# Optimization experiments

Measured on AMD Instinct MI355X. Metric: run time of the kernel, lower is better.

The kernel has to match this reference:

```python
import jax, jax.numpy as jnp
import numpy as np

N_NODES = 100000
N_EDGES = 600000
N_GRAPHS = 5000
IN_DIM = 11
HID = 128
EDGE_DIM = 3
N_REST = 4  # layers 1..4
BN_EPS = 1e-5


def setup_inputs() -> dict:
    key = jax.random.key(0)
    ks = iter(jax.random.split(key, 40))
    s = 0.05
    inp = {}
    inp['x'] = jax.random.normal(next(ks), (N_NODES, IN_DIM), dtype=jnp.float32)
    inp['edge_attr'] = jax.random.normal(next(ks), (N_EDGES, EDGE_DIM), dtype=jnp.float32)
    # layer 0 (input_dim -> hidden)
    inp['e_w0'] = jax.random.normal(next(ks), (EDGE_DIM, IN_DIM), dtype=jnp.float32) * s
    inp['e_b0'] = jnp.zeros((IN_DIM,), jnp.float32)
    inp['w1_0'] = jax.random.normal(next(ks), (IN_DIM, HID), dtype=jnp.float32) * s
    inp['b1_0'] = jnp.zeros((HID,), jnp.float32)
    inp['w2_0'] = jax.random.normal(next(ks), (HID, HID), dtype=jnp.float32) * s
    inp['b2_0'] = jnp.zeros((HID,), jnp.float32)
    inp['gamma0'] = jnp.ones((HID,), jnp.float32)
    inp['beta0'] = jnp.zeros((HID,), jnp.float32)
    inp['eps0'] = jnp.zeros((), jnp.float32)
    # layers 1..4 stacked
    inp['e_w'] = jax.random.normal(next(ks), (N_REST, EDGE_DIM, HID), dtype=jnp.float32) * s
    inp['e_b'] = jnp.zeros((N_REST, HID), jnp.float32)
    inp['w1'] = jax.random.normal(next(ks), (N_REST, HID, HID), dtype=jnp.float32) * s
    inp['b1'] = jnp.zeros((N_REST, HID), jnp.float32)
    inp['w2'] = jax.random.normal(next(ks), (N_REST, HID, HID), dtype=jnp.float32) * s
    inp['b2'] = jnp.zeros((N_REST, HID), jnp.float32)
    inp['gamma'] = jnp.ones((N_REST, HID), jnp.float32)
    inp['beta'] = jnp.zeros((N_REST, HID), jnp.float32)
    inp['eps_r'] = jnp.zeros((N_REST,), jnp.float32)
    # head MLP
    inp['hw1'] = jax.random.normal(next(ks), (HID, HID), dtype=jnp.float32) * s
    inp['hb1'] = jnp.zeros((HID,), jnp.float32)
    inp['hw2'] = jax.random.normal(next(ks), (HID, HID), dtype=jnp.float32) * s
    inp['hb2'] = jnp.zeros((HID,), jnp.float32)
    inp['hw3'] = jax.random.normal(next(ks), (HID, 1), dtype=jnp.float32) * s
    inp['hb3'] = jnp.zeros((1,), jnp.float32)
    # graph structure (int constants)
    inp['edge_index'] = jax.random.randint(next(ks), (2, N_EDGES), 0, N_NODES, dtype=jnp.int32)
    inp['batch'] = jnp.sort(jax.random.randint(next(ks), (N_NODES,), 0, N_GRAPHS, dtype=jnp.int32))
    return inp


def _gine_layer(x, src, dst, edge_attr, e_w, e_b, eps, w1, b1, w2, b2, gamma, beta):
    # message = relu(x_j + Linear(edge_attr)); aggregate = scatter-add on dst
    msg = jax.nn.relu(x[src] + edge_attr @ e_w + e_b)            # [E, d]
    aggr = jax.ops.segment_sum(msg, dst, num_segments=N_NODES)  # [N, d]
    h = (1.0 + eps) * x + aggr
    h = jax.nn.relu(h @ w1 + b1) @ w2 + b2                       # GIN MLP
    mu = h.mean(axis=0)
    var = h.var(axis=0)  # biased, as torch BN training-mode normalization
    h = (h - mu) * jax.lax.rsqrt(var + BN_EPS) * gamma + beta
    return jax.nn.relu(h)


def reference(x, edge_attr, e_w0, e_b0, w1_0, b1_0, w2_0, b2_0, gamma0, beta0, eps0,
              e_w, e_b, w1, b1, w2, b2, gamma, beta, eps_r,
              hw1, hb1, hw2, hb2, hw3, hb3, edge_index, batch):
    src, dst = edge_index[0], edge_index[1]
    # layer 0: input_dim -> hidden, no residual (dims differ)
    h = _gine_layer(x, src, dst, edge_attr, e_w0, e_b0, eps0,
                    w1_0, b1_0, w2_0, b2_0, gamma0, beta0)
    # layers 1..4: hidden -> hidden, with residual
    for i in range(N_REST):
        h_res = h
        h = _gine_layer(h, src, dst, edge_attr, e_w[i], e_b[i], eps_r[i],
                        w1[i], b1[i], w2[i], b2[i], gamma[i], beta[i])
        h = h + h_res
    # global mean pool per graph
    sums = jax.ops.segment_sum(h, batch, num_segments=N_GRAPHS)
    cnts = jax.ops.segment_sum(jnp.ones((h.shape[0],), h.dtype), batch, num_segments=N_GRAPHS)
    pooled = sums / jnp.maximum(cnts, 1.0)[:, None]
    # head MLP (dropout = eval no-op)
    z = jax.nn.relu(pooled @ hw1 + hb1)
    z = jax.nn.relu(z @ hw2 + hb2)
    return z @ hw3 + hb3
```

## Files before the change

### kernel.cpp

```cpp
#include <hip/hip_runtime.h>
#include <hip/hip_fp16.h>

#define N_NODES 100000
#define N_EDGES 600000
#define N_GRAPHS 5000
#define IN_DIM 11
#define HID 128
#define NREST 4
#define BN_EPS 1e-5f
#define SCAN_BS 256
#define NBLK ((N_NODES + SCAN_BS - 1) / SCAN_BS)
#define WSLOT 16384

typedef __bf16 bf16x8 __attribute__((ext_vector_type(8)));
typedef float f32x4 __attribute__((ext_vector_type(4)));

__device__ inline bf16x8 as_bf16x8(uint4 u) { return __builtin_bit_cast(bf16x8, u); }

__device__ inline void split_bf16(float x, unsigned short& hi, unsigned short& lo) {
    unsigned int b = __float_as_uint(x);
    hi = (unsigned short)(b >> 16);
    float rem = x - __uint_as_float(b & 0xFFFF0000u);
    lo = (unsigned short)(__float_as_uint(rem) >> 16);
}

__device__ inline uint4 pack8(const unsigned short* h) {
    uint4 u;
    u.x = (unsigned)h[0] | ((unsigned)h[1] << 16);
    u.y = (unsigned)h[2] | ((unsigned)h[3] << 16);
    u.z = (unsigned)h[4] | ((unsigned)h[5] << 16);
    u.w = (unsigned)h[6] | ((unsigned)h[7] << 16);
    return u;
}

__global__ void k_zero(int* deg, int* gstart, int* gend, float* stats) {
    int i = blockIdx.x * 256 + threadIdx.x;
    if (i < N_NODES) deg[i] = 0;
    if (i < N_GRAPHS) { gstart[i] = 0; gend[i] = 0; }
    if (i < 5 * 2 * HID) stats[i] = 0.f;
}

__global__ void k_deg(const int* __restrict__ ei, int* __restrict__ deg) {
    int e = blockIdx.x * 256 + threadIdx.x;
    if (e < N_EDGES) atomicAdd(&deg[ei[N_EDGES + e]], 1);
}

__global__ void k_scan_a(const int* __restrict__ deg, int* __restrict__ rowstart,
                         int* __restrict__ bsum) {
    __shared__ int sh[SCAN_BS];
    int t = threadIdx.x, i = blockIdx.x * SCAN_BS + t;
    int v = (i < N_NODES) ? deg[i] : 0;
    sh[t] = v;
    __syncthreads();
    for (int off = 1; off < SCAN_BS; off <<= 1) {
        int add = (t >= off) ? sh[t - off] : 0;
        __syncthreads();
        sh[t] += add;
        __syncthreads();
    }
    if (i < N_NODES) rowstart[i] = sh[t] - v;
    if (t == SCAN_BS - 1) bsum[blockIdx.x] = sh[t];
}

__global__ void k_scan_b(const int* __restrict__ bsum, int* __restrict__ boff) {
    __shared__ int sh[512];
    int t = threadIdx.x;
    int v = (t < NBLK) ? bsum[t] : 0;
    sh[t] = v;
    __syncthreads();
    for (int off = 1; off < 512; off <<= 1) {
        int add = (t >= off) ? sh[t - off] : 0;
        __syncthreads();
        sh[t] += add;
        __syncthreads();
    }
    if (t < NBLK) boff[t] = sh[t] - v;
}

__global__ void k_scan_c(int* __restrict__ rowstart, const int* __restrict__ boff,
                         int* __restrict__ cur) {
    int i = blockIdx.x * 256 + threadIdx.x;
    if (i < N_NODES) {
        int v = rowstart[i] + boff[i / SCAN_BS];
        rowstart[i] = v;
        cur[i] = v;
    }
    if (i == 0) rowstart[N_NODES] = N_EDGES;
}

__global__ void k_fill(const int* __restrict__ ei, const float* __restrict__ ea,
                       int* __restrict__ cur, int* __restrict__ csr_src,
                       float* __restrict__ csr_ea) {
    int e = blockIdx.x * 256 + threadIdx.x;
    if (e < N_EDGES) {
        int d = ei[N_EDGES + e];
        int p = atomicAdd(&cur[d], 1);
        csr_src[p] = ei[e];
        csr_ea[3 * p + 0] = ea[3 * e + 0];
        csr_ea[3 * p + 1] = ea[3 * e + 1];
        csr_ea[3 * p + 2] = ea[3 * e + 2];
    }
}

__global__ void k_pack(const float* __restrict__ w1_0, const float* __restrict__ w2_0,
                       const float* __restrict__ w1, const float* __restrict__ w2,
                       unsigned short* __restrict__ Whi, unsigned short* __restrict__ Wlo) {
    int bid = blockIdx.x;
    int slot = bid >> 5;
    int kc = (bid >> 3) & 3, cb = bid & 7;
    int lane = threadIdx.x;
    const float* src;
    int K;
    if (slot == 0) { src = w1_0; K = IN_DIM; }
    else if (slot == 1) { src = w2_0; K = HID; }
    else if (slot < 6) { src = w1 + (size_t)(slot - 2) * HID * HID; K = HID; }
    else { src = w2 + (size_t)(slot - 6) * HID * HID; K = HID; }
    int col = cb * 16 + (lane & 15);
    int kbase = kc * 32 + 8 * (lane >> 4);
    unsigned short hi[8], lo[8];
#pragma unroll
    for (int j = 0; j < 8; ++j) {
        int k = kbase + j;
        float v = (k < K) ? src[(size_t)k * HID + col] : 0.f;
        split_bf16(v, hi[j], lo[j]);
    }
    size_t base = ((size_t)bid * 64 + lane) * 8;
    *(uint4*)(Whi + base) = pack8(hi);
    *(uint4*)(Wlo + base) = pack8(lo);
}

__global__ void k_agg0(const float* __restrict__ x, const int* __restrict__ rowstart,
                       const int* __restrict__ csr_src, const float* __restrict__ csr_ea,
                       const float* __restrict__ ew, const float* __restrict__ eb,
                       const float* __restrict__ epsp, float* __restrict__ Z0) {
    int wave = (blockIdx.x * blockDim.x + threadIdx.x) >> 6;
    int lane = threadIdx.x & 63;
    if (wave >= N_NODES) return;
    int n = wave;
    int slot = lane >> 4;
    int c = lane & 15;
    int cc = (c < IN_DIM) ? c : 0;
    float w0 = ew[0 * IN_DIM + cc], w1 = ew[1 * IN_DIM + cc], w2 = ew[2 * IN_DIM + cc];
    float bb = eb[cc];
    float acc = 0.f;
    int i0 = rowstart[n], i1 = rowstart[n + 1];
    for (int i = i0 + slot; i < i1; i += 4) {
        int s = csr_src[i];
        float ea0 = csr_ea[3 * i], ea1 = csr_ea[3 * i + 1], ea2 = csr_ea[3 * i + 2];
        float m = x[s * IN_DIM + cc] + ea0 * w0 + ea1 * w1 + ea2 * w2 + bb;
        acc += fmaxf(m, 0.f);
    }
    acc += __shfl_xor(acc, 16, 64);
    acc += __shfl_xor(acc, 32, 64);
    if (lane < IN_DIM) {
        float epsv = 1.0f + epsp[0];
        Z0[n * IN_DIM + lane] = epsv * x[n * IN_DIM + lane] + acc;
    }
}

__global__ void k_agg128(const float* __restrict__ h, const __half* __restrict__ hh,
                         const int* __restrict__ rowstart,
                         const int* __restrict__ csr_src, const float* __restrict__ csr_ea,
                         const float* __restrict__ ew, const float* __restrict__ eb,
                         const float* __restrict__ epsp, int layer, float* __restrict__ Z) {
    int wave = (blockIdx.x * blockDim.x + threadIdx.x) >> 6;
    int lane = threadIdx.x & 63;
    if (wave >= N_NODES) return;
    int n = wave;
    int slot = lane >> 4;
    int c = (lane & 15) * 8;
    float4 w0a = *(const float4*)(ew + 0 * HID + c), w0b = *(const float4*)(ew + 0 * HID + c + 4);
    float4 w1a = *(const float4*)(ew + 1 * HID + c), w1b = *(const float4*)(ew + 1 * HID + c + 4);
    float4 w2a = *(const float4*)(ew + 2 * HID + c), w2b = *(const float4*)(ew + 2 * HID + c + 4);
    float4 bba = *(const float4*)(eb + c),           bbb = *(const float4*)(eb + c + 4);
    float a0 = 0.f, a1 = 0.f, a2 = 0.f, a3 = 0.f, a4 = 0.f, a5 = 0.f, a6 = 0.f, a7 = 0.f;
    int i0 = rowstart[n], i1 = rowstart[n + 1];
    for (int i = i0 + slot; i < i1; i += 4) {
        int s = csr_src[i];
        float ea0 = csr_ea[3 * i], ea1 = csr_ea[3 * i + 1], ea2 = csr_ea[3 * i + 2];
        uint4 hv = *(const uint4*)(hh + (size_t)s * HID + c);
        float2 f0 = __half22float2(__builtin_bit_cast(__half2, hv.x));
        float2 f1 = __half22float2(__builtin_bit_cast(__half2, hv.y));
        float2 f2 = __half22float2(__builtin_bit_cast(__half2, hv.z));
        float2 f3 = __half22float2(__builtin_bit_cast(__half2, hv.w));
        a0 += fmaxf(f0.x + ea0 * w0a.x + ea1 * w1a.x + ea2 * w2a.x + bba.x, 0.f);
        a1 += fmaxf(f0.y + ea0 * w0a.y + ea1 * w1a.y + ea2 * w2a.y + bba.y, 0.f);
        a2 += fmaxf(f1.x + ea0 * w0a.z + ea1 * w1a.z + ea2 * w2a.z + bba.z, 0.f);
        a3 += fmaxf(f1.y + ea0 * w0a.w + ea1 * w1a.w + ea2 * w2a.w + bba.w, 0.f);
        a4 += fmaxf(f2.x + ea0 * w0b.x + ea1 * w1b.x + ea2 * w2b.x + bbb.x, 0.f);
        a5 += fmaxf(f2.y + ea0 * w0b.y + ea1 * w1b.y + ea2 * w2b.y + bbb.y, 0.f);
        a6 += fmaxf(f3.x + ea0 * w0b.z + ea1 * w1b.z + ea2 * w2b.z + bbb.z, 0.f);
        a7 += fmaxf(f3.y + ea0 * w0b.w + ea1 * w1b.w + ea2 * w2b.w + bbb.w, 0.f);
    }
#pragma unroll
    for (int m = 16; m <= 32; m <<= 1) {
        a0 += __shfl_xor(a0, m, 64); a1 += __shfl_xor(a1, m, 64);
        a2 += __shfl_xor(a2, m, 64); a3 += __shfl_xor(a3, m, 64);
        a4 += __shfl_xor(a4, m, 64); a5 += __shfl_xor(a5, m, 64);
        a6 += __shfl_xor(a6, m, 64); a7 += __shfl_xor(a7, m, 64);
    }
    if (slot == 0) {
        float epsv = 1.0f + epsp[layer];
        float4 hna = *(const float4*)(h + (size_t)n * HID + c);
        float4 hnb = *(const float4*)(h + (size_t)n * HID + c + 4);
        float4 za, zb;
        za.x = epsv * hna.x + a0; za.y = epsv * hna.y + a1;
        za.z = epsv * hna.z + a2; za.w = epsv * hna.w + a3;
        zb.x = epsv * hnb.x + a4; zb.y = epsv * hnb.y + a5;
        zb.z = epsv * hnb.z + a6; zb.w = epsv * hnb.w + a7;
        *(float4*)(Z + (size_t)n * HID + c) = za;
        *(float4*)(Z + (size_t)n * HID + c + 4) = zb;
    }
}

template <int K1>
__global__ __launch_bounds__(256, 4) void k_mlp(const float* Zin,
        const unsigned short* __restrict__ W1hi, const unsigned short* __restrict__ W1lo,
        const unsigned short* __restrict__ W2hi, const unsigned short* __restrict__ W2lo,
        const float* __restrict__ B1, const float* __restrict__ B2,
        float* Hpre, float* __restrict__ stats) {
    constexpr int KC1 = (K1 == 128) ? 4 : 1;
    __shared__ __align__(16) unsigned short ahi[4 * 4 * 64 * 8];
    __shared__ __align__(16) unsigned short alo[4 * 4 * 64 * 8];
    __shared__ float red[1024];
    const int tid = threadIdx.x;
    const int w = tid >> 6;
    const int l = tid & 63;
    const int row0 = blockIdx.x * 64;

    if (K1 == 128) {
#pragma unroll
        for (int it = 0; it < 4; ++it) {
            int s = tid + it * 256;
            int lane = s & 63, kc = (s >> 6) & 3, wr = s >> 8;
            int r = row0 + wr * 16 + (lane & 15);
            int k0 = kc * 32 + 8 * (lane >> 4);
            float v[8];
            if (r < N_NODES) {
                *(float4*)(v) = *(const float4*)(Zin + (size_t)r * 128 + k0);
                *(float4*)(v + 4) = *(const float4*)(Zin + (size_t)r * 128 + k0 + 4);
            } else {
#pragma unroll
                for (int j = 0; j < 8; ++j) v[j] = 0.f;
            }
            unsigned short h[8], q[8];
#pragma unroll
            for (int j = 0; j < 8; ++j) split_bf16(v[j], h[j], q[j]);
            *(uint4*)(ahi + (size_t)s * 8) = pack8(h);
            *(uint4*)(alo + (size_t)s * 8) = pack8(q);
        }
    } else {
        int lane = tid & 63, wr = tid >> 6;
        int r = row0 + wr * 16 + (lane & 15);
        int k0 = 8 * (lane >> 4);
        float v[8];
#pragma unroll
        for (int j = 0; j < 8; ++j) {
            int k = k0 + j;
            v[j] = (r < N_NODES && k < IN_DIM) ? Zin[(size_t)r * IN_DIM + k] : 0.f;
        }
        unsigned short h[8], q[8];
#pragma unroll
        for (int j = 0; j < 8; ++j) split_bf16(v[j], h[j], q[j]);
        size_t s = (size_t)(wr * 4 + 0) * 64 + lane;
        *(uint4*)(ahi + s * 8) = pack8(h);
        *(uint4*)(alo + s * 8) = pack8(q);
    }
    __syncthreads();

    const int cb0 = 2 * w, cb1 = cb0 + 1;
    const f32x4 zf = {0.f, 0.f, 0.f, 0.f};

    f32x4 acc[4][2];
#pragma unroll
    for (int wr = 0; wr < 4; ++wr) { acc[wr][0] = zf; acc[wr][1] = zf; }

#pragma unroll
    for (int kc = 0; kc < KC1; ++kc) {
        bf16x8 bh0 = as_bf16x8(*(const uint4*)(W1hi + ((size_t)(kc * 8 + cb0) * 64 + l) * 8));
        bf16x8 bl0 = as_bf16x8(*(const uint4*)(W1lo + ((size_t)(kc * 8 + cb0) * 64 + l) * 8));
        bf16x8 bh1 = as_bf16x8(*(const uint4*)(W1hi + ((size_t)(kc * 8 + cb1) * 64 + l) * 8));
        bf16x8 bl1 = as_bf16x8(*(const uint4*)(W1lo + ((size_t)(kc * 8 + cb1) * 64 + l) * 8));
#pragma unroll
        for (int wr = 0; wr < 4; ++wr) {
            bf16x8 a_h = as_bf16x8(*(const uint4*)(ahi + ((size_t)(wr * 4 + kc) * 64 + l) * 8));
            bf16x8 a_l = as_bf16x8(*(const uint4*)(alo + ((size_t)(wr * 4 + kc) * 64 + l) * 8));
            acc[wr][0] = __builtin_amdgcn_mfma_f32_16x16x32_bf16(a_h, bh0, acc[wr][0], 0, 0, 0);
            acc[wr][1] = __builtin_amdgcn_mfma_f32_16x16x32_bf16(a_h, bh1, acc[wr][1], 0, 0, 0);
            acc[wr][0] = __builtin_amdgcn_mfma_f32_16x16x32_bf16(a_l, bh0, acc[wr][0], 0, 0, 0);
            acc[wr][1] = __builtin_amdgcn_mfma_f32_16x16x32_bf16(a_l, bh1, acc[wr][1], 0, 0, 0);
            acc[wr][0] = __builtin_amdgcn_mfma_f32_16x16x32_bf16(a_h, bl0, acc[wr][0], 0, 0, 0);
            acc[wr][1] = __builtin_amdgcn_mfma_f32_16x16x32_bf16(a_h, bl1, acc[wr][1], 0, 0, 0);
        }
    }
    __syncthreads();

    {
        float b1c0 = B1[cb0 * 16 + (l & 15)];
        float b1c1 = B1[cb1 * 16 + (l & 15)];
        int j2 = l & 7;
        int hi16 = (l & 15) >> 3;
        int l2r = (l >> 4) * 4;
#pragma unroll
        for (int wr = 0; wr < 4; ++wr) {
#pragma unroll
            for (int cbl = 0; cbl < 2; ++cbl) {
                float bv = cbl ? b1c1 : b1c0;
                f32x4 v = acc[wr][cbl];
#pragma unroll
                for (int r = 0; r < 4; ++r) {
                    float t = fmaxf(v[r] + bv, 0.f);
                    unsigned short hh, qq;
                    split_bf16(t, hh, qq);
                    int l2 = l2r + r + 16 * (2 * cbl + hi16);
                    int off = ((wr * 4 + w) * 64 + l2) * 8 + j2;
                    ahi[off] = hh;
                    alo[off] = qq;
                }
            }
        }
    }
    __syncthreads();

    f32x4 acc2[4][2];
#pragma unroll
    for (int wr = 0; wr < 4; ++wr) { acc2[wr][0] = zf; acc2[wr][1] = zf; }

#pragma unroll
    for (int kc = 0; kc < 4; ++kc) {
        bf16x8 bh0 = as_bf16x8(*(const uint4*)(W2hi + ((size_t)(kc * 8 + cb0) * 64 + l) * 8));
        bf16x8 bl0 = as_bf16x8(*(const uint4*)(W2lo + ((size_t)(kc * 8 + cb0) * 64 + l) * 8));
        bf16x8 bh1 = as_bf16x8(*(const uint4*)(W2hi + ((size_t)(kc * 8 + cb1) * 64 + l) * 8));
        bf16x8 bl1 = as_bf16x8(*(const uint4*)(W2lo + ((size_t)(kc * 8 + cb1) * 64 + l) * 8));
#pragma unroll
        for (int wr = 0; wr < 4; ++wr) {
            bf16x8 a_h = as_bf16x8(*(const uint4*)(ahi + ((size_t)(wr * 4 + kc) * 64 + l) * 8));
            bf16x8 a_l = as_bf16x8(*(const uint4*)(alo + ((size_t)(wr * 4 + kc) * 64 + l) * 8));
            acc2[wr][0] = __builtin_amdgcn_mfma_f32_16x16x32_bf16(a_h, bh0, acc2[wr][0], 0, 0, 0);
            acc2[wr][1] = __builtin_amdgcn_mfma_f32_16x16x32_bf16(a_h, bh1, acc2[wr][1], 0, 0, 0);
            acc2[wr][0] = __builtin_amdgcn_mfma_f32_16x16x32_bf16(a_l, bh0, acc2[wr][0], 0, 0, 0);
            acc2[wr][1] = __builtin_amdgcn_mfma_f32_16x16x32_bf16(a_l, bh1, acc2[wr][1], 0, 0, 0);
            acc2[wr][0] = __builtin_amdgcn_mfma_f32_16x16x32_bf16(a_h, bl0, acc2[wr][0], 0, 0, 0);
            acc2[wr][1] = __builtin_amdgcn_mfma_f32_16x16x32_bf16(a_h, bl1, acc2[wr][1], 0, 0, 0);
        }
    }

    {
        float b2c0 = B2[cb0 * 16 + (l & 15)];
        float b2c1 = B2[cb1 * 16 + (l & 15)];
        float s0 = 0.f, q0 = 0.f, s1 = 0.f, q1 = 0.f;
#pragma unroll
        for (int wr = 0; wr < 4; ++wr) {
#pragma unroll
            for (int r = 0; r < 4; ++r) {
                int grow = row0 + wr * 16 + (l >> 4) * 4 + r;
                if (grow < N_NODES) {
                    float o0 = acc2[wr][0][r] + b2c0;
                    float o1 = acc2[wr][1][r] + b2c1;
                    Hpre[(size_t)grow * 128 + cb0 * 16 + (l & 15)] = o0;
                    Hpre[(size_t)grow * 128 + cb1 * 16 + (l & 15)] = o1;
                    s0 += o0; q0 += o0 * o0;
                    s1 += o1; q1 += o1 * o1;
                }
            }
        }
        red[(w * 2 + 0) * 64 + l] = s0;
        red[(w * 2 + 1) * 64 + l] = s1;
        red[512 + (w * 2 + 0) * 64 + l] = q0;
        red[512 + (w * 2 + 1) * 64 + l] = q1;
    }
    __syncthreads();
    if (tid < 128) {
        int b = ((tid >> 5) * 2 + ((tid >> 4) & 1)) * 64 + (tid & 15);
        float ss = red[b] + red[b + 16] + red[b + 32] + red[b + 48];
        float qq = red[512 + b] + red[512 + b + 16] + red[512 + b + 32] + red[512 + b + 48];
        atomicAdd(&stats[tid], ss);
        atomicAdd(&stats[128 + tid], qq);
    }
}

__global__ void k_bn(const float* __restrict__ Hpre, const float* __restrict__ stats,
                     const float* __restrict__ gamma, const float* __restrict__ beta,
                     float* __restrict__ h, __half* __restrict__ hh, int residual) {
    int idx = blockIdx.x * 256 + threadIdx.x;
    const float invN = 1.f / (float)N_NODES;
    int c4 = idx & 31;
    float4 v = ((const float4*)Hpre)[idx];
    float4 s0 = ((const float4*)stats)[c4];
    float4 s1 = ((const float4*)(stats + 128))[c4];
    float4 g = ((const float4*)gamma)[c4];
    float4 bt = ((const float4*)beta)[c4];
    float4 r;
    {
        float mu = s0.x * invN, var = s1.x * invN - mu * mu;
        r.x = fmaxf((v.x - mu) * rsqrtf(var + BN_EPS) * g.x + bt.x, 0.f);
    }
    {
        float mu = s0.y * invN, var = s1.y * invN - mu * mu;
        r.y = fmaxf((v.y - mu) * rsqrtf(var + BN_EPS) * g.y + bt.y, 0.f);
    }
    {
        float mu = s0.z * invN, var = s1.z * invN - mu * mu;
        r.z = fmaxf((v.z - mu) * rsqrtf(var + BN_EPS) * g.z + bt.z, 0.f);
    }
    {
        float mu = s0.w * invN, var = s1.w * invN - mu * mu;
        r.w = fmaxf((v.w - mu) * rsqrtf(var + BN_EPS) * g.w + bt.w, 0.f);
    }
    if (residual) {
        float4 hv = ((const float4*)h)[idx];
        r.x += hv.x; r.y += hv.y; r.z += hv.z; r.w += hv.w;
    }
    ((float4*)h)[idx] = r;
    if (hh) {
        __half2 p0 = __floats2half2_rn(r.x, r.y);
        __half2 p1 = __floats2half2_rn(r.z, r.w);
        uint2 pk;
        pk.x = __builtin_bit_cast(unsigned int, p0);
        pk.y = __builtin_bit_cast(unsigned int, p1);
        *(uint2*)(hh + (size_t)idx * 4) = pk;
    }
}

__global__ void k_bounds(const int* __restrict__ batch, int* __restrict__ gstart,
                         int* __restrict__ gend) {
    int r = blockIdx.x * 256 + threadIdx.x;
    if (r >= N_NODES) return;
    int b = batch[r];
    if (r == 0 || batch[r - 1] != b) gstart[b] = r;
    if (r == N_NODES - 1 || batch[r + 1] != b) gend[b] = r + 1;
}

__global__ void k_pool(const float* __restrict__ h, const int* __restrict__ gstart,
                       const int* __restrict__ gend, float* __restrict__ pooled) {
    int wave = (blockIdx.x * blockDim.x + threadIdx.x) >> 6;
    int lane = threadIdx.x & 63;
    if (wave >= N_GRAPHS) return;
    int g = wave;
    int c = lane * 2;
    int a = gstart[g], b = gend[g];
    float ax = 0.f, ay = 0.f;
    for (int r = a; r < b; ++r) {
        float2 v = *(const float2*)(h + (size_t)r * HID + c);
        ax += v.x;
        ay += v.y;
    }
    float d = fmaxf((float)(b - a), 1.f);
    float2 o;
    o.x = ax / d;
    o.y = ay / d;
    *(float2*)(pooled + (size_t)g * HID + c) = o;
}

__global__ void k_head(const float* __restrict__ pooled, const float* __restrict__ hw1,
                       const float* __restrict__ hb1, const float* __restrict__ hw2,
                       const float* __restrict__ hb2, const float* __restrict__ hw3,
                       const float* __restrict__ hb3, float* __restrict__ out) {
    __shared__ float ps[2][128];
    __shared__ float t1s[2][128];
    __shared__ float red[256];
    int tid = threadIdx.x;
    int rr = tid >> 7, c = tid & 127;
    int row = blockIdx.x * 2 + rr;
    ps[rr][c] = pooled[(size_t)row * 128 + c];
    __syncthreads();
    float a = hb1[c];
    for (int k = 0; k < 128; ++k) a = fmaf(ps[rr][k], hw1[k * 128 + c], a);
    t1s[rr][c] = fmaxf(a, 0.f);
    __syncthreads();
    float b = hb2[c];
    for (int k = 0; k < 128; ++k) b = fmaf(t1s[rr][k], hw2[k * 128 + c], b);
    b = fmaxf(b, 0.f);
    red[tid] = b * hw3[c];
    for (int s = 64; s > 0; s >>= 1) {
        __syncthreads();
        if (c < s) red[tid] += red[tid + s];
    }
    __syncthreads();
    if (c == 0) out[row] = red[tid] + hb3[0];
}

extern "C" void kernel_launch(void* const* d_in, const int* in_sizes, int n_in,
                              void* d_out, int out_size, void* d_ws, size_t ws_size,
                              hipStream_t stream) {
    const float* x = (const float*)d_in[0];
    const float* edge_attr = (const float*)d_in[1];
    const float* e_w0 = (const float*)d_in[2];
    const float* e_b0 = (const float*)d_in[3];
    const float* w1_0 = (const float*)d_in[4];
    const float* b1_0 = (const float*)d_in[5];
    const float* w2_0 = (const float*)d_in[6];
    const float* b2_0 = (const float*)d_in[7];
    const float* gamma0 = (const float*)d_in[8];
    const float* beta0 = (const float*)d_in[9];
    const float* eps0 = (const float*)d_in[10];
    const float* e_w = (const float*)d_in[11];
    const float* e_b = (const float*)d_in[12];
    const float* w1 = (const float*)d_in[13];
    const float* b1 = (const float*)d_in[14];
    const float* w2 = (const float*)d_in[15];
    const float* b2 = (const float*)d_in[16];
    const float* gamma = (const float*)d_in[17];
    const float* beta = (const float*)d_in[18];
    const float* eps_r = (const float*)d_in[19];
    const float* hw1 = (const float*)d_in[20];
    const float* hb1 = (const float*)d_in[21];
    const float* hw2 = (const float*)d_in[22];
    const float* hb2 = (const float*)d_in[23];
    const float* hw3 = (const float*)d_in[24];
    const float* hb3 = (const float*)d_in[25];
    const int* edge_index = (const int*)d_in[26];
    const int* batch = (const int*)d_in[27];
    float* out = (float*)d_out;

    float* wsf = (float*)d_ws;
    size_t off = 0;
    float* A = wsf + off;      off += (size_t)N_NODES * HID;
    float* ZB = wsf + off;     off += (size_t)N_NODES * HID;
    float* Z0 = wsf + off;     off += (size_t)N_NODES * IN_DIM;
    float* pooled = wsf + off; off += (size_t)N_GRAPHS * HID;
    float* stats = wsf + off;  off += 5 * 2 * HID;
    float* csr_ea = wsf + off; off += (size_t)3 * N_EDGES;
    __half* hhalf = (__half*)(wsf + off); off += (size_t)N_NODES * HID / 2;
    int* ib = (int*)(wsf + off);
    size_t io = 0;
    int* deg = ib + io;      io += N_NODES;
    int* rowstart = ib + io; io += N_NODES + 4;
    int* cur = ib + io;      io += N_NODES;
    int* csr_src = ib + io;  io += N_EDGES;
    int* gstart = ib + io;   io += N_GRAPHS;
    int* gend = ib + io;     io += N_GRAPHS;
    int* bsum = ib + io;     io += 512;
    int* boff = ib + io;     io += 512;
    unsigned short* Whi = (unsigned short*)(ib + io);
    unsigned short* Wlo = Whi + 10 * WSLOT;

    const int EB = (N_EDGES + 255) / 256;
    const int NB = (N_NODES + 255) / 256;
    const int MLPB = (N_NODES + 63) / 64;

    k_zero<<<NB, 256, 0, stream>>>(deg, gstart, gend, stats);
    k_pack<<<320, 64, 0, stream>>>(w1_0, w2_0, w1, w2, Whi, Wlo);

    k_deg<<<EB, 256, 0, stream>>>(edge_index, deg);
    k_scan_a<<<NBLK, SCAN_BS, 0, stream>>>(deg, rowstart, bsum);
    k_scan_b<<<1, 512, 0, stream>>>(bsum, boff);
    k_scan_c<<<NB, 256, 0, stream>>>(rowstart, boff, cur);
    k_fill<<<EB, 256, 0, stream>>>(edge_index, edge_attr, cur, csr_src, csr_ea);

    k_agg0<<<(N_NODES * 64) / 256, 256, 0, stream>>>(x, rowstart, csr_src, csr_ea, e_w0,
                                                     e_b0, eps0, Z0);
    k_mlp<IN_DIM><<<MLPB, 256, 0, stream>>>(Z0, Whi + 0 * WSLOT, Wlo + 0 * WSLOT,
                                            Whi + 1 * WSLOT, Wlo + 1 * WSLOT,
                                            b1_0, b2_0, ZB, stats);
    k_bn<<<(N_NODES * HID / 4) / 256, 256, 0, stream>>>(ZB, stats, gamma0, beta0, A,
                                                        hhalf, 0);

    for (int i = 0; i < NREST; ++i) {
        k_agg128<<<(N_NODES * 64) / 256, 256, 0, stream>>>(
            A, hhalf, rowstart, csr_src, csr_ea, e_w + (size_t)i * 3 * HID,
            e_b + (size_t)i * HID, eps_r, i, ZB);
        k_mlp<HID><<<MLPB, 256, 0, stream>>>(ZB, Whi + (size_t)(2 + i) * WSLOT,
                                             Wlo + (size_t)(2 + i) * WSLOT,
                                             Whi + (size_t)(6 + i) * WSLOT,
                                             Wlo + (size_t)(6 + i) * WSLOT,
                                             b1 + (size_t)i * HID, b2 + (size_t)i * HID,
                                             ZB, stats + (size_t)(i + 1) * 2 * HID);
        k_bn<<<(N_NODES * HID / 4) / 256, 256, 0, stream>>>(
            ZB, stats + (size_t)(i + 1) * 2 * HID, gamma + (size_t)i * HID,
            beta + (size_t)i * HID, A, (i < NREST - 1) ? hhalf : (__half*)nullptr, 1);
    }

    k_bounds<<<NB, 256, 0, stream>>>(batch, gstart, gend);
    k_pool<<<(N_GRAPHS * 64) / 256, 256, 0, stream>>>(A, gstart, gend, pooled);
    k_head<<<N_GRAPHS / 2, 256, 0, stream>>>(pooled, hw1, hb1, hw2, hb2, hw3, hb3, out);
}
```

Measured before the change: 901.5 us.

## Pack CSR edge data into uint4 and process 8 edges per wave in aggregation

Packs each CSR edge's source index and three edge attributes into one 16-byte record, so the aggregation kernels issue a single vector load per edge instead of four scalar loads. k_agg128 is reworked so each wave handles 8 edges at once with 16 channels per lane, which should raise memory-level parallelism for the gather. The cost is more accumulator and weight registers per lane, a deeper shuffle reduction, and a workspace layout change that moves the packed edges to the start of the integer region.

```diff
diff --git a/kernel.cpp b/kernel.cpp
--- a/kernel.cpp
+++ b/kernel.cpp
@@ -89,16 +89,17 @@
 }
 
 __global__ void k_fill(const int* __restrict__ ei, const float* __restrict__ ea,
-                       int* __restrict__ cur, int* __restrict__ csr_src,
-                       float* __restrict__ csr_ea) {
+                       int* __restrict__ cur, uint4* __restrict__ csr_pack) {
     int e = blockIdx.x * 256 + threadIdx.x;
     if (e < N_EDGES) {
         int d = ei[N_EDGES + e];
         int p = atomicAdd(&cur[d], 1);
-        csr_src[p] = ei[e];
-        csr_ea[3 * p + 0] = ea[3 * e + 0];
-        csr_ea[3 * p + 1] = ea[3 * e + 1];
-        csr_ea[3 * p + 2] = ea[3 * e + 2];
+        uint4 pk;
+        pk.x = (unsigned)ei[e];
+        pk.y = __float_as_uint(ea[3 * e + 0]);
+        pk.z = __float_as_uint(ea[3 * e + 1]);
+        pk.w = __float_as_uint(ea[3 * e + 2]);
+        csr_pack[p] = pk;
     }
 }
 
@@ -130,7 +131,7 @@
 }
 
 __global__ void k_agg0(const float* __restrict__ x, const int* __restrict__ rowstart,
-                       const int* __restrict__ csr_src, const float* __restrict__ csr_ea,
+                       const uint4* __restrict__ csr_pack,
                        const float* __restrict__ ew, const float* __restrict__ eb,
                        const float* __restrict__ epsp, float* __restrict__ Z0) {
     int wave = (blockIdx.x * blockDim.x + threadIdx.x) >> 6;
@@ -140,14 +141,15 @@
     int slot = lane >> 4;
     int c = lane & 15;
     int cc = (c < IN_DIM) ? c : 0;
-    float w0 = ew[0 * IN_DIM + cc], w1 = ew[1 * IN_DIM + cc], w2 = ew[2 * IN_DIM + cc];
+    float w0 = ew[cc], w1 = ew[IN_DIM + cc], w2 = ew[2 * IN_DIM + cc];
     float bb = eb[cc];
     float acc = 0.f;
     int i0 = rowstart[n], i1 = rowstart[n + 1];
     for (int i = i0 + slot; i < i1; i += 4) {
-        int s = csr_src[i];
-        float ea0 = csr_ea[3 * i], ea1 = csr_ea[3 * i + 1], ea2 = csr_ea[3 * i + 2];
-        float m = x[s * IN_DIM + cc] + ea0 * w0 + ea1 * w1 + ea2 * w2 + bb;
+        uint4 pk = csr_pack[i];
+        int s = (int)pk.x;
+        float m = x[s * IN_DIM + cc] + __uint_as_float(pk.y) * w0 +
+                  __uint_as_float(pk.z) * w1 + __uint_as_float(pk.w) * w2 + bb;
         acc += fmaxf(m, 0.f);
     }
     acc += __shfl_xor(acc, 16, 64);
@@ -158,58 +160,66 @@
     }
 }
 
-__global__ void k_agg128(const float* __restrict__ h, const __half* __restrict__ hh,
-                         const int* __restrict__ rowstart,
-                         const int* __restrict__ csr_src, const float* __restrict__ csr_ea,
-                         const float* __restrict__ ew, const float* __restrict__ eb,
-                         const float* __restrict__ epsp, int layer, float* __restrict__ Z) {
+__global__ __launch_bounds__(256, 4) void k_agg128(
+        const float* __restrict__ h, const __half* __restrict__ hh,
+        const int* __restrict__ rowstart, const uint4* __restrict__ csr_pack,
+        const float* __restrict__ ew, const float* __restrict__ eb,
+        const float* __restrict__ epsp, int layer, float* __restrict__ Z) {
     int wave = (blockIdx.x * blockDim.x + threadIdx.x) >> 6;
     int lane = threadIdx.x & 63;
     if (wave >= N_NODES) return;
     int n = wave;
-    int slot = lane >> 4;
-    int c = (lane & 15) * 8;
-    float4 w0a = *(const float4*)(ew + 0 * HID + c), w0b = *(const float4*)(ew + 0 * HID + c + 4);
-    float4 w1a = *(const float4*)(ew + 1 * HID + c), w1b = *(const float4*)(ew + 1 * HID + c + 4);
-    float4 w2a = *(const float4*)(ew + 2 * HID + c), w2b = *(const float4*)(ew + 2 * HID + c + 4);
-    float4 bba = *(const float4*)(eb + c),           bbb = *(const float4*)(eb + c + 4);
-    float a0 = 0.f, a1 = 0.f, a2 = 0.f, a3 = 0.f, a4 = 0.f, a5 = 0.f, a6 = 0.f, a7 = 0.f;
+    int slot = lane >> 3;
+    int c = (lane & 7) * 16;
+    float4 W0[4], W1[4], W2[4], BB[4];
+#pragma unroll
+    for (int q = 0; q < 4; ++q) {
+        W0[q] = *(const float4*)(ew + 0 * HID + c + 4 * q);
+        W1[q] = *(const float4*)(ew + 1 * HID + c + 4 * q);
+        W2[q] = *(const float4*)(ew + 2 * HID + c + 4 * q);
+        BB[q] = *(const float4*)(eb + c + 4 * q);
+    }
+    float A[16];
+#pragma unroll
+    for (int j = 0; j < 16; ++j) A[j] = 0.f;
     int i0 = rowstart[n], i1 = rowstart[n + 1];
-    for (int i = i0 + slot; i < i1; i += 4) {
-        int s = csr_src[i];
-        float ea0 = csr_ea[3 * i], ea1 = csr_ea[3 * i + 1], ea2 = csr_ea[3 * i + 2];
-        uint4 hv = *(const uint4*)(hh + (size_t)s * HID + c);
-        float2 f0 = __half22float2(__builtin_bit_cast(__half2, hv.x));
-        float2 f1 = __half22float2(__builtin_bit_cast(__half2, hv.y));
-        float2 f2 = __half22float2(__builtin_bit_cast(__half2, hv.z));
-        float2 f3 = __half22float2(__builtin_bit_cast(__half2, hv.w));
-        a0 += fmaxf(f0.x + ea0 * w0a.x + ea1 * w1a.x + ea2 * w2a.x + bba.x, 0.f);
-        a1 += fmaxf(f0.y + ea0 * w0a.y + ea1 * w1a.y + ea2 * w2a.y + bba.y, 0.f);
-        a2 += fmaxf(f1.x + ea0 * w0a.z + ea1 * w1a.z + ea2 * w2a.z + bba.z, 0.f);
-        a3 += fmaxf(f1.y + ea0 * w0a.w + ea1 * w1a.w + ea2 * w2a.w + bba.w, 0.f);
-        a4 += fmaxf(f2.x + ea0 * w0b.x + ea1 * w1b.x + ea2 * w2b.x + bbb.x, 0.f);
-        a5 += fmaxf(f2.y + ea0 * w0b.y + ea1 * w1b.y + ea2 * w2b.y + bbb.y, 0.f);
-        a6 += fmaxf(f3.x + ea0 * w0b.z + ea1 * w1b.z + ea2 * w2b.z + bbb.z, 0.f);
-        a7 += fmaxf(f3.y + ea0 * w0b.w + ea1 * w1b.w + ea2 * w2b.w + bbb.w, 0.f);
-    }
-#pragma unroll
-    for (int m = 16; m <= 32; m <<= 1) {
-        a0 += __shfl_xor(a0, m, 64); a1 += __shfl_xor(a1, m, 64);
-        a2 += __shfl_xor(a2, m, 64); a3 += __shfl_xor(a3, m, 64);
-        a4 += __shfl_xor(a4, m, 64); a5 += __shfl_xor(a5, m, 64);
-        a6 += __shfl_xor(a6, m, 64); a7 += __shfl_xor(a7, m, 64);
-    }
-    if (slot == 0) {
+    for (int i = i0 + slot; i < i1; i += 8) {
+        uint4 pk = csr_pack[i];
+        int s = (int)pk.x;
+        float ea0 = __uint_as_float(pk.y);
+        float ea1 = __uint_as_float(pk.z);
+        float ea2 = __uint_as_float(pk.w);
+        uint4 hv0 = *(const uint4*)(hh + (size_t)s * HID + c);
+        uint4 hv1 = *(const uint4*)(hh + (size_t)s * HID + c + 8);
+        unsigned hu[8] = {hv0.x, hv0.y, hv0.z, hv0.w, hv1.x, hv1.y, hv1.z, hv1.w};
+#pragma unroll
+        for (int q = 0; q < 4; ++q) {
+            float2 fa = __half22float2(__builtin_bit_cast(__half2, hu[2 * q]));
+            float2 fb = __half22float2(__builtin_bit_cast(__half2, hu[2 * q + 1]));
+            A[4 * q + 0] += fmaxf(fa.x + ea0 * W0[q].x + ea1 * W1[q].x + ea2 * W2[q].x + BB[q].x, 0.f);
+            A[4 * q + 1] += fmaxf(fa.y + ea0 * W0[q].y + ea1 * W1[q].y + ea2 * W2[q].y + BB[q].y, 0.f);
+            A[4 * q + 2] += fmaxf(fb.x + ea0 * W0[q].z + ea1 * W1[q].z + ea2 * W2[q].z + BB[q].z, 0.f);
+            A[4 * q + 3] += fmaxf(fb.y + ea0 * W0[q].w + ea1 * W1[q].w + ea2 * W2[q].w + BB[q].w, 0.f);
+        }
+    }
+#pragma unroll
+    for (int j = 0; j < 16; ++j) {
+        A[j] += __shfl_xor(A[j], 8, 64);
+        A[j] += __shfl_xor(A[j], 16, 64);
+        A[j] += __shfl_xor(A[j], 32, 64);
+    }
+    if (lane < 8) {
         float epsv = 1.0f + epsp[layer];
-        float4 hna = *(const float4*)(h + (size_t)n * HID + c);
-        float4 hnb = *(const float4*)(h + (size_t)n * HID + c + 4);
-        float4 za, zb;
-        za.x = epsv * hna.x + a0; za.y = epsv * hna.y + a1;
-        za.z = epsv * hna.z + a2; za.w = epsv * hna.w + a3;
-        zb.x = epsv * hnb.x + a4; zb.y = epsv * hnb.y + a5;
-        zb.z = epsv * hnb.z + a6; zb.w = epsv * hnb.w + a7;
-        *(float4*)(Z + (size_t)n * HID + c) = za;
-        *(float4*)(Z + (size_t)n * HID + c + 4) = zb;
+#pragma unroll
+        for (int q = 0; q < 4; ++q) {
+            float4 hn = *(const float4*)(h + (size_t)n * HID + c + 4 * q);
+            float4 z;
+            z.x = epsv * hn.x + A[4 * q + 0];
+            z.y = epsv * hn.y + A[4 * q + 1];
+            z.z = epsv * hn.z + A[4 * q + 2];
+            z.w = epsv * hn.w + A[4 * q + 3];
+            *(float4*)(Z + (size_t)n * HID + c + 4 * q) = z;
+        }
     }
 }
 
@@ -520,14 +530,13 @@
     float* Z0 = wsf + off;     off += (size_t)N_NODES * IN_DIM;
     float* pooled = wsf + off; off += (size_t)N_GRAPHS * HID;
     float* stats = wsf + off;  off += 5 * 2 * HID;
-    float* csr_ea = wsf + off; off += (size_t)3 * N_EDGES;
     __half* hhalf = (__half*)(wsf + off); off += (size_t)N_NODES * HID / 2;
     int* ib = (int*)(wsf + off);
-    size_t io = 0;
+    uint4* csr_pack = (uint4*)ib;
+    size_t io = 4 * (size_t)N_EDGES;
     int* deg = ib + io;      io += N_NODES;
     int* rowstart = ib + io; io += N_NODES + 4;
     int* cur = ib + io;      io += N_NODES;
-    int* csr_src = ib + io;  io += N_EDGES;
     int* gstart = ib + io;   io += N_GRAPHS;
     int* gend = ib + io;     io += N_GRAPHS;
     int* bsum = ib + io;     io += 512;
@@ -546,9 +555,9 @@
     k_scan_a<<<NBLK, SCAN_BS, 0, stream>>>(deg, rowstart, bsum);
     k_scan_b<<<1, 512, 0, stream>>>(bsum, boff);
     k_scan_c<<<NB, 256, 0, stream>>>(rowstart, boff, cur);
-    k_fill<<<EB, 256, 0, stream>>>(edge_index, edge_attr, cur, csr_src, csr_ea);
-
-    k_agg0<<<(N_NODES * 64) / 256, 256, 0, stream>>>(x, rowstart, csr_src, csr_ea, e_w0,
+    k_fill<<<EB, 256, 0, stream>>>(edge_index, edge_attr, cur, csr_pack);
+
+    k_agg0<<<(N_NODES * 64) / 256, 256, 0, stream>>>(x, rowstart, csr_pack, e_w0,
                                                      e_b0, eps0, Z0);
     k_mlp<IN_DIM><<<MLPB, 256, 0, stream>>>(Z0, Whi + 0 * WSLOT, Wlo + 0 * WSLOT,
                                             Whi + 1 * WSLOT, Wlo + 1 * WSLOT,
@@ -558,7 +567,7 @@
 
     for (int i = 0; i < NREST; ++i) {
         k_agg128<<<(N_NODES * 64) / 256, 256, 0, stream>>>(
-            A, hhalf, rowstart, csr_src, csr_ea, e_w + (size_t)i * 3 * HID,
+            A, hhalf, rowstart, csr_pack, e_w + (size_t)i * 3 * HID,
             e_b + (size_t)i * HID, eps_r, i, ZB);
         k_mlp<HID><<<MLPB, 256, 0, stream>>>(ZB, Whi + (size_t)(2 + i) * WSLOT,
                                              Wlo + (size_t)(2 + i) * WSLOT,
```

Measured after the change: 1.171 ms. +29.9%, slower.

## Pack CSR source and edge attributes into uint4 and prefetch next edge

Applied to the files above, without the earlier changes.

Merges the separate csr_src and csr_ea arrays into one 16-byte record per edge, so each edge in the aggregation kernels needs a single vector load instead of four scalar loads. Both aggregation loops now software-prefetch the next edge record before processing the current one, and k_agg128 gets a launch bounds hint. The cost is a slightly larger CSR footprint (16 vs 16 bytes, essentially equal) and extra registers for the prefetched record.

```diff
diff --git a/kernel.cpp b/kernel.cpp
--- a/kernel.cpp
+++ b/kernel.cpp
@@ -89,16 +89,17 @@
 }
 
 __global__ void k_fill(const int* __restrict__ ei, const float* __restrict__ ea,
-                       int* __restrict__ cur, int* __restrict__ csr_src,
-                       float* __restrict__ csr_ea) {
+                       int* __restrict__ cur, uint4* __restrict__ csr_pack) {
     int e = blockIdx.x * 256 + threadIdx.x;
     if (e < N_EDGES) {
         int d = ei[N_EDGES + e];
         int p = atomicAdd(&cur[d], 1);
-        csr_src[p] = ei[e];
-        csr_ea[3 * p + 0] = ea[3 * e + 0];
-        csr_ea[3 * p + 1] = ea[3 * e + 1];
-        csr_ea[3 * p + 2] = ea[3 * e + 2];
+        uint4 pk;
+        pk.x = (unsigned)ei[e];
+        pk.y = __float_as_uint(ea[3 * e + 0]);
+        pk.z = __float_as_uint(ea[3 * e + 1]);
+        pk.w = __float_as_uint(ea[3 * e + 2]);
+        csr_pack[p] = pk;
     }
 }
 
@@ -130,7 +131,7 @@
 }
 
 __global__ void k_agg0(const float* __restrict__ x, const int* __restrict__ rowstart,
-                       const int* __restrict__ csr_src, const float* __restrict__ csr_ea,
+                       const uint4* __restrict__ csr_pack,
                        const float* __restrict__ ew, const float* __restrict__ eb,
                        const float* __restrict__ epsp, float* __restrict__ Z0) {
     int wave = (blockIdx.x * blockDim.x + threadIdx.x) >> 6;
@@ -140,15 +141,23 @@
     int slot = lane >> 4;
     int c = lane & 15;
     int cc = (c < IN_DIM) ? c : 0;
-    float w0 = ew[0 * IN_DIM + cc], w1 = ew[1 * IN_DIM + cc], w2 = ew[2 * IN_DIM + cc];
+    float w0 = ew[cc], w1 = ew[IN_DIM + cc], w2 = ew[2 * IN_DIM + cc];
     float bb = eb[cc];
     float acc = 0.f;
     int i0 = rowstart[n], i1 = rowstart[n + 1];
-    for (int i = i0 + slot; i < i1; i += 4) {
-        int s = csr_src[i];
-        float ea0 = csr_ea[3 * i], ea1 = csr_ea[3 * i + 1], ea2 = csr_ea[3 * i + 2];
-        float m = x[s * IN_DIM + cc] + ea0 * w0 + ea1 * w1 + ea2 * w2 + bb;
+    int i = i0 + slot;
+    uint4 pk;
+    if (i < i1) pk = csr_pack[i];
+    while (i < i1) {
+        int inext = i + 4;
+        uint4 pknext;
+        if (inext < i1) pknext = csr_pack[inext];
+        int s = (int)pk.x;
+        float m = x[s * IN_DIM + cc] + __uint_as_float(pk.y) * w0 +
+                  __uint_as_float(pk.z) * w1 + __uint_as_float(pk.w) * w2 + bb;
         acc += fmaxf(m, 0.f);
+        pk = pknext;
+        i = inext;
     }
     acc += __shfl_xor(acc, 16, 64);
     acc += __shfl_xor(acc, 32, 64);
@@ -158,11 +167,11 @@
     }
 }
 
-__global__ void k_agg128(const float* __restrict__ h, const __half* __restrict__ hh,
-                         const int* __restrict__ rowstart,
-                         const int* __restrict__ csr_src, const float* __restrict__ csr_ea,
-                         const float* __restrict__ ew, const float* __restrict__ eb,
-                         const float* __restrict__ epsp, int layer, float* __restrict__ Z) {
+__global__ __launch_bounds__(256, 4) void k_agg128(
+        const float* __restrict__ h, const __half* __restrict__ hh,
+        const int* __restrict__ rowstart, const uint4* __restrict__ csr_pack,
+        const float* __restrict__ ew, const float* __restrict__ eb,
+        const float* __restrict__ epsp, int layer, float* __restrict__ Z) {
     int wave = (blockIdx.x * blockDim.x + threadIdx.x) >> 6;
     int lane = threadIdx.x & 63;
     if (wave >= N_NODES) return;
@@ -175,9 +184,17 @@
     float4 bba = *(const float4*)(eb + c),           bbb = *(const float4*)(eb + c + 4);
     float a0 = 0.f, a1 = 0.f, a2 = 0.f, a3 = 0.f, a4 = 0.f, a5 = 0.f, a6 = 0.f, a7 = 0.f;
     int i0 = rowstart[n], i1 = rowstart[n + 1];
-    for (int i = i0 + slot; i < i1; i += 4) {
-        int s = csr_src[i];
-        float ea0 = csr_ea[3 * i], ea1 = csr_ea[3 * i + 1], ea2 = csr_ea[3 * i + 2];
+    int i = i0 + slot;
+    uint4 pk;
+    if (i < i1) pk = csr_pack[i];
+    while (i < i1) {
+        int inext = i + 4;
+        uint4 pknext;
+        if (inext < i1) pknext = csr_pack[inext];
+        int s = (int)pk.x;
+        float ea0 = __uint_as_float(pk.y);
+        float ea1 = __uint_as_float(pk.z);
+        float ea2 = __uint_as_float(pk.w);
         uint4 hv = *(const uint4*)(hh + (size_t)s * HID + c);
         float2 f0 = __half22float2(__builtin_bit_cast(__half2, hv.x));
         float2 f1 = __half22float2(__builtin_bit_cast(__half2, hv.y));
@@ -191,6 +208,8 @@
         a5 += fmaxf(f2.y + ea0 * w0b.y + ea1 * w1b.y + ea2 * w2b.y + bbb.y, 0.f);
         a6 += fmaxf(f3.x + ea0 * w0b.z + ea1 * w1b.z + ea2 * w2b.z + bbb.z, 0.f);
         a7 += fmaxf(f3.y + ea0 * w0b.w + ea1 * w1b.w + ea2 * w2b.w + bbb.w, 0.f);
+        pk = pknext;
+        i = inext;
     }
 #pragma unroll
     for (int m = 16; m <= 32; m <<= 1) {
@@ -520,14 +539,13 @@
     float* Z0 = wsf + off;     off += (size_t)N_NODES * IN_DIM;
     float* pooled = wsf + off; off += (size_t)N_GRAPHS * HID;
     float* stats = wsf + off;  off += 5 * 2 * HID;
-    float* csr_ea = wsf + off; off += (size_t)3 * N_EDGES;
     __half* hhalf = (__half*)(wsf + off); off += (size_t)N_NODES * HID / 2;
     int* ib = (int*)(wsf + off);
-    size_t io = 0;
+    uint4* csr_pack = (uint4*)ib;
+    size_t io = 4 * (size_t)N_EDGES;
     int* deg = ib + io;      io += N_NODES;
     int* rowstart = ib + io; io += N_NODES + 4;
     int* cur = ib + io;      io += N_NODES;
-    int* csr_src = ib + io;  io += N_EDGES;
     int* gstart = ib + io;   io += N_GRAPHS;
     int* gend = ib + io;     io += N_GRAPHS;
     int* bsum = ib + io;     io += 512;
@@ -546,9 +564,9 @@
     k_scan_a<<<NBLK, SCAN_BS, 0, stream>>>(deg, rowstart, bsum);
     k_scan_b<<<1, 512, 0, stream>>>(bsum, boff);
     k_scan_c<<<NB, 256, 0, stream>>>(rowstart, boff, cur);
-    k_fill<<<EB, 256, 0, stream>>>(edge_index, edge_attr, cur, csr_src, csr_ea);
-
-    k_agg0<<<(N_NODES * 64) / 256, 256, 0, stream>>>(x, rowstart, csr_src, csr_ea, e_w0,
+    k_fill<<<EB, 256, 0, stream>>>(edge_index, edge_attr, cur, csr_pack);
+
+    k_agg0<<<(N_NODES * 64) / 256, 256, 0, stream>>>(x, rowstart, csr_pack, e_w0,
                                                      e_b0, eps0, Z0);
     k_mlp<IN_DIM><<<MLPB, 256, 0, stream>>>(Z0, Whi + 0 * WSLOT, Wlo + 0 * WSLOT,
                                             Whi + 1 * WSLOT, Wlo + 1 * WSLOT,
@@ -558,7 +576,7 @@
 
     for (int i = 0; i < NREST; ++i) {
         k_agg128<<<(N_NODES * 64) / 256, 256, 0, stream>>>(
-            A, hhalf, rowstart, csr_src, csr_ea, e_w + (size_t)i * 3 * HID,
+            A, hhalf, rowstart, csr_pack, e_w + (size_t)i * 3 * HID,
             e_b + (size_t)i * HID, eps_r, i, ZB);
         k_mlp<HID><<<MLPB, 256, 0, stream>>>(ZB, Whi + (size_t)(2 + i) * WSLOT,
                                              Wlo + (size_t)(2 + i) * WSLOT,
```

Result: slower. 920.3 us (+2.1%).
